# Optimization experiments

Hardware: AMD Instinct MI355X
Metric: run time of the kernel (lower is better)

The kernel has to match this reference:

```python
import jax, jax.numpy as jnp
import numpy as np

N = 100000
E = 1600000
D = 128
LAYERS = 2


def setup_inputs() -> dict:
    key = jax.random.key(0)
    k1, k2, k3, k4, k5, k6 = jax.random.split(key, 6)
    features = jax.random.normal(k1, (N, D), dtype=jnp.float32)
    edge_row = jax.random.randint(k2, (E,), 0, N)
    edge_col = jax.random.randint(k3, (E,), 0, N)
    edge_val = jax.random.uniform(k4, (E,), dtype=jnp.float32)
    # new_features[index] = out_features with out_features having N rows =>
    # index is a permutation covering all N nodes
    index = jax.random.permutation(k5, N)
    a_in = jax.random.normal(k6, (3,), dtype=jnp.float32)
    return {"features": features, "edge_row": edge_row, "edge_col": edge_col,
            "edge_val": edge_val, "index": index, "a_in": a_in}


def reference(features, edge_row, edge_col, edge_val, index, a_in):
    n, d = features.shape
    # --- normalize_adj: D^{-1/2} A D^{-1/2} (Mat is constant across layers) ---
    rowsum = jax.ops.segment_sum(edge_val, edge_row, num_segments=n)  # [N]
    d_inv_sqrt = jnp.where(rowsum > 0, rowsum ** -0.5, 0.0)
    vals = d_inv_sqrt[edge_row] * edge_val * d_inv_sqrt[edge_col]      # [E]

    # softmax over first Layers+1 entries of a_in
    a = jax.nn.softmax(a_in[:LAYERS + 1])

    # nodes covered by index keep the SpMM result; others keep old features
    covered = jnp.zeros((n,), dtype=bool).at[index].set(True)

    result = a[0] * features
    h = features
    for j in range(LAYERS):
        # SpMM: out[r] = sum_e vals[e] * h[col[e]] for row[e] == r
        out = jax.ops.segment_sum(vals[:, None] * h[edge_col], edge_row,
                                  num_segments=n)                      # [N, D]
        scattered = jnp.zeros_like(h).at[index].set(out)
        h = jnp.where(covered[:, None], scattered, h)
        result = result + a[j + 1] * h
    return result
```

## Files before the change

kernel.cpp:

```cpp
#include <hip/hip_runtime.h>

#define WPB    4
#define SCAN_B 1024
#define P1B    256
#define BKT_SH 8

typedef unsigned u32x4 __attribute__((ext_vector_type(4)));
typedef float    f32x4 __attribute__((ext_vector_type(4)));
typedef float    f32x2 __attribute__((ext_vector_type(2)));

__device__ __forceinline__ unsigned bf16rne(float x) {
  unsigned u = __float_as_uint(x);
  return (u + 0x7fffu + ((u >> 16) & 1u)) >> 16;
}
__device__ __forceinline__ float bf_lo(unsigned g) { return __uint_as_float(g << 16); }
__device__ __forceinline__ float bf_hi(unsigned g) { return __uint_as_float(g & 0xffff0000u); }

__global__ void prep_p1_k(const f32x2* __restrict__ f, unsigned* __restrict__ hb, int nw,
                          const float* __restrict__ a_in, float* __restrict__ a_buf,
                          const int* __restrict__ index, int* __restrict__ covered,
                          int* __restrict__ row_start, const int* __restrict__ erow,
                          int* __restrict__ bhist, int E, int N, int C, int NB) {
  extern __shared__ int h[];
  const bool dop1 = (blockIdx.x < P1B);
  if (dop1) {
    for (int k = threadIdx.x; k < NB; k += 256) h[k] = 0;
    __syncthreads();
  }
  int i = blockIdx.x * 256 + threadIdx.x;
  if (i < nw) {
    f32x2 v = __builtin_nontemporal_load(f + i);
    hb[i] = bf16rne(v.x) | (bf16rne(v.y) << 16);
  }
  if (i < N) covered[index[i]] = 1;
  if (i == 0) {
    row_start[N] = E;
    float x0 = a_in[0], x1 = a_in[1], x2 = a_in[2];
    float m = fmaxf(x0, fmaxf(x1, x2));
    float e0 = expf(x0 - m), e1 = expf(x1 - m), e2 = expf(x2 - m);
    float s = e0 + e1 + e2;
    a_buf[0] = e0 / s; a_buf[1] = e1 / s; a_buf[2] = e2 / s;
  }
  if (dop1) {
    int s = blockIdx.x * C, e = min(E, s + C);
    for (int j = s + threadIdx.x; j < e; j += 256)
      atomicAdd(&h[erow[j] >> BKT_SH], 1);
    __syncthreads();
    for (int k = threadIdx.x; k < NB; k += 256)
      bhist[(size_t)k * P1B + blockIdx.x] = h[k];
  }
}

__global__ void scanA_k(const int* __restrict__ cnt, int* __restrict__ incl,
                        int* __restrict__ bsum, int n) {
  __shared__ int tmp[SCAN_B];
  int tid = threadIdx.x;
  int g = blockIdx.x * SCAN_B + tid;
  tmp[tid] = (g < n) ? cnt[g] : 0;
  __syncthreads();
  for (int off = 1; off < SCAN_B; off <<= 1) {
    int t = (tid >= off) ? tmp[tid - off] : 0;
    __syncthreads();
    tmp[tid] += t;
    __syncthreads();
  }
  if (g < n) incl[g] = tmp[tid];
  if (tid == SCAN_B - 1) bsum[blockIdx.x] = tmp[tid];
}

__global__ void scanBC_k(int* __restrict__ boffs, const int* __restrict__ bhist,
                         const int* __restrict__ bsum, int nb, int n) {
  __shared__ int bs[128];
  int tid = threadIdx.x;
  if (tid < 128) bs[tid] = (tid < nb) ? bsum[tid] : 0;
  __syncthreads();
  for (int off = 1; off < 128; off <<= 1) {
    int t = (tid >= off && tid < 128) ? bs[tid - off] : 0;
    __syncthreads();
    if (tid < 128) bs[tid] += t;
    __syncthreads();
  }
  int g = blockIdx.x * SCAN_B + tid;
  if (g < n) {
    int off2 = (blockIdx.x > 0) ? bs[blockIdx.x - 1] : 0;
    boffs[g] = boffs[g] + off2 - bhist[g];
  }
}

__global__ void p2_k(const int* __restrict__ row, const int* __restrict__ col,
                     const float* __restrict__ val, const int* __restrict__ boffs,
                     int2* __restrict__ bedge, int E, int C, int NB) {
  extern __shared__ int cur[];
  for (int k = threadIdx.x; k < NB; k += 256)
    cur[k] = boffs[(size_t)k * P1B + blockIdx.x];
  __syncthreads();
  int s = blockIdx.x * C, e = min(E, s + C);
  for (int i = s + threadIdx.x; i < e; i += 256) {
    int r = row[i];
    int p = atomicAdd(&cur[r >> BKT_SH], 1);
    bedge[p] = make_int2(((r & 255) << 24) | col[i], __float_as_int(val[i]));
  }
}

__global__ void p3_k(const int2* __restrict__ bedge, const int* __restrict__ boffs,
                     int* __restrict__ row_start, float* __restrict__ dis,
                     int2* __restrict__ pairs, int E, int N, int NB) {
  __shared__ int rcnt[256];
  __shared__ float rsum[256];
  __shared__ int rbase[256];
  __shared__ int tmp[256];
  int kb = blockIdx.x, t = threadIdx.x;
  int base = boffs[(size_t)kb * P1B];
  int end  = (kb + 1 < NB) ? boffs[(size_t)(kb + 1) * P1B] : E;
  rcnt[t] = 0; rsum[t] = 0.f;
  __syncthreads();
  for (int i = base + t; i < end; i += 256) {
    int2 p = bedge[i];
    int rlo = ((unsigned)p.x) >> 24;
    atomicAdd(&rcnt[rlo], 1);
    atomicAdd(&rsum[rlo], __int_as_float(p.y));
  }
  __syncthreads();
  int v = rcnt[t];
  tmp[t] = v;
  __syncthreads();
  for (int off = 1; off < 256; off <<= 1) {
    int u = (t >= off) ? tmp[t - off] : 0;
    __syncthreads();
    tmp[t] += u;
    __syncthreads();
  }
  rbase[t] = tmp[t] - v;
  int r = (kb << BKT_SH) + t;
  if (r < N) {
    row_start[r] = base + rbase[t];
    float s = rsum[t];
    dis[r] = (s > 0.0f) ? rsqrtf(s) : 0.0f;
  }
  __syncthreads();
  rcnt[t] = rbase[t];
  __syncthreads();
  for (int i = base + t; i < end; i += 256) {
    int2 p = bedge[i];
    int rlo = ((unsigned)p.x) >> 24;
    int pos = base + atomicAdd(&rcnt[rlo], 1);
    pairs[pos] = make_int2(p.x & 0xFFFFFF, p.y);
  }
}

__device__ __forceinline__ void acc8(float v, u32x4 g, float* a) {
  a[0] = fmaf(v, bf_lo(g.x), a[0]); a[1] = fmaf(v, bf_hi(g.x), a[1]);
  a[2] = fmaf(v, bf_lo(g.y), a[2]); a[3] = fmaf(v, bf_hi(g.y), a[3]);
  a[4] = fmaf(v, bf_lo(g.z), a[4]); a[5] = fmaf(v, bf_hi(g.z), a[5]);
  a[6] = fmaf(v, bf_lo(g.w), a[6]); a[7] = fmaf(v, bf_hi(g.w), a[7]);
}

__device__ __forceinline__ void spmm_body(const int* __restrict__ row_start,
                                          const int2* __restrict__ pairs,
                                          const float* __restrict__ dis,
                                          const char* __restrict__ hb,
                                          int wave, int lane, float* a) {
  int q = lane >> 4;
  unsigned qoff = (unsigned)(lane & 15) << 4;
  int beg = row_start[wave], end = row_start[wave + 1];
  for (int base = beg; base < end; base += 64) {
    unsigned long long pl = 0;
    if (base + lane < end)
      pl = __builtin_nontemporal_load((const unsigned long long*)(pairs + base + lane));
    int pc = (int)(pl & 0xffffffffu);
    float pv = __uint_as_float((unsigned)(pl >> 32)) * dis[pc];
    int m = end - base; if (m > 64) m = 64;
    for (int j = 0; j < m; j += 16) {
      int   c0 = __shfl(pc, j + q),      c1 = __shfl(pc, j + 4 + q);
      int   c2 = __shfl(pc, j + 8 + q),  c3 = __shfl(pc, j + 12 + q);
      float v0 = __shfl(pv, j + q),      v1 = __shfl(pv, j + 4 + q);
      float v2 = __shfl(pv, j + 8 + q),  v3 = __shfl(pv, j + 12 + q);
      u32x4 g0 = *(const u32x4*)(hb + (((unsigned)c0 << 8) | qoff));
      u32x4 g1 = *(const u32x4*)(hb + (((unsigned)c1 << 8) | qoff));
      u32x4 g2 = *(const u32x4*)(hb + (((unsigned)c2 << 8) | qoff));
      u32x4 g3 = *(const u32x4*)(hb + (((unsigned)c3 << 8) | qoff));
      acc8(v0, g0, a); acc8(v1, g1, a);
      acc8(v2, g2, a); acc8(v3, g3, a);
    }
  }
#pragma unroll
  for (int i = 0; i < 8; ++i) a[i] += __shfl_xor(a[i], 16);
#pragma unroll
  for (int i = 0; i < 8; ++i) a[i] += __shfl_xor(a[i], 32);
}

__global__ void spmm1_k(const int* __restrict__ row_start, const int2* __restrict__ pairs,
                        const float* __restrict__ dis, const unsigned* __restrict__ hB,
                        const int* __restrict__ index, u32x4* __restrict__ hA4, int n) {
  int wave = blockIdx.x * WPB + (threadIdx.x >> 6);
  if (wave >= n) return;
  int lane = threadIdx.x & 63;
  float a[8] = {0.f, 0.f, 0.f, 0.f, 0.f, 0.f, 0.f, 0.f};
  spmm_body(row_start, pairs, dis, (const char*)hB, wave, lane, a);
  if ((lane >> 4) == 0) {
    float dr = dis[wave];
    u32x4 pk;
    pk.x = bf16rne(a[0] * dr) | (bf16rne(a[1] * dr) << 16);
    pk.y = bf16rne(a[2] * dr) | (bf16rne(a[3] * dr) << 16);
    pk.z = bf16rne(a[4] * dr) | (bf16rne(a[5] * dr) << 16);
    pk.w = bf16rne(a[6] * dr) | (bf16rne(a[7] * dr) << 16);
    hA4[(unsigned)index[wave] * 16u + (unsigned)(lane & 15)] = pk;
  }
}

__global__ void spmm2_k(const int* __restrict__ row_start, const int2* __restrict__ pairs,
                        const float* __restrict__ dis, const u32x4* __restrict__ hA4,
                        const u32x4* __restrict__ hB4, const int* __restrict__ index,
                        f32x4* __restrict__ out4, const float* __restrict__ ac, int n) {
  int wave = blockIdx.x * WPB + (threadIdx.x >> 6);
  if (wave >= n) return;
  int lane = threadIdx.x & 63;
  float a[8] = {0.f, 0.f, 0.f, 0.f, 0.f, 0.f, 0.f, 0.f};
  spmm_body(row_start, pairs, dis, (const char*)hA4, wave, lane, a);
  if ((lane >> 4) == 0) {
    unsigned ql = lane & 15;
    float dr = dis[wave];
    unsigned ro = (unsigned)index[wave] * 16u + ql;
    u32x4 ga = hA4[ro];
    u32x4 gb = __builtin_nontemporal_load(hB4 + ro);
    float c0 = ac[0], c1 = ac[1], c2 = ac[2];
    f32x4 w0, w1;
    w0.x = fmaf(c2, a[0] * dr, fmaf(c1, bf_lo(ga.x), c0 * bf_lo(gb.x)));
    w0.y = fmaf(c2, a[1] * dr, fmaf(c1, bf_hi(ga.x), c0 * bf_hi(gb.x)));
    w0.z = fmaf(c2, a[2] * dr, fmaf(c1, bf_lo(ga.y), c0 * bf_lo(gb.y)));
    w0.w = fmaf(c2, a[3] * dr, fmaf(c1, bf_hi(ga.y), c0 * bf_hi(gb.y)));
    w1.x = fmaf(c2, a[4] * dr, fmaf(c1, bf_lo(ga.z), c0 * bf_lo(gb.z)));
    w1.y = fmaf(c2, a[5] * dr, fmaf(c1, bf_hi(ga.z), c0 * bf_hi(gb.z)));
    w1.z = fmaf(c2, a[6] * dr, fmaf(c1, bf_lo(ga.w), c0 * bf_lo(gb.w)));
    w1.w = fmaf(c2, a[7] * dr, fmaf(c1, bf_hi(ga.w), c0 * bf_hi(gb.w)));
    unsigned ob = (unsigned)index[wave] * 32u + 2u * ql;
    __builtin_nontemporal_store(w0, out4 + ob);
    __builtin_nontemporal_store(w1, out4 + ob + 1);
  }
}

__global__ void fixup1_k(const int* __restrict__ covered, const u32x4* __restrict__ hB4,
                         u32x4* __restrict__ hA4, int n) {
  int v = blockIdx.x * 256 + threadIdx.x;
  if (v >= n || covered[v]) return;
  for (int d = 0; d < 16; ++d) hA4[(size_t)v * 16 + d] = hB4[(size_t)v * 16 + d];
}

__global__ void fixup2_k(const int* __restrict__ covered, const float2* __restrict__ feat,
                         float2* __restrict__ out, const float* __restrict__ a, int n) {
  int v = blockIdx.x * 256 + threadIdx.x;
  if (v >= n || covered[v]) return;
  float s = a[0] + a[1] + a[2];
  for (int d = 0; d < 64; ++d) {
    float2 f = feat[(size_t)v * 64 + d];
    out[(size_t)v * 64 + d] = make_float2(s * f.x, s * f.y);
  }
}

extern "C" void kernel_launch(void* const* d_in, const int* in_sizes, int n_in,
                              void* d_out, int out_size, void* d_ws, size_t ws_size,
                              hipStream_t stream) {
  const float* features = (const float*)d_in[0];
  const int*   edge_row = (const int*)d_in[1];
  const int*   edge_col = (const int*)d_in[2];
  const float* edge_val = (const float*)d_in[3];
  const int*   index    = (const int*)d_in[4];
  const float* a_in     = (const float*)d_in[5];

  const int E = in_sizes[1];
  const int N = in_sizes[4];
  const int NB = (N + 255) >> BKT_SH;
  const int NBH = NB * P1B;
  const int C = (E + P1B - 1) / P1B;

  float* out = (float*)d_out;

  char* ws = (char*)d_ws;
  size_t off = 0;
  auto carve = [&](size_t bytes) -> char* {
    char* p = ws + off;
    off = (off + bytes + 255) & ~(size_t)255;
    return p;
  };
  float* a_buf     = (float*)carve(16 * sizeof(float));
  float* dis       = (float*)carve((size_t)N * 4);
  int*   covered   = (int*)carve((size_t)N * 4);
  int*   row_start = (int*)carve((size_t)(N + 1) * 4);
  int*   bsum      = (int*)carve(256 * 4);
  int2*  pairs     = (int2*)carve((size_t)E * 8);
  unsigned* hB     = (unsigned*)carve((size_t)N * 64 * 4);
  size_t ov_bytes = (size_t)NBH * 4 * 2 + (size_t)E * 8 + 1024;
  size_t hA_bytes = (size_t)N * 64 * 4;
  char* ovl = carve(ov_bytes > hA_bytes ? ov_bytes : hA_bytes);
  int*  bhist = (int*)ovl;
  int*  boffs = (int*)(ovl + (((size_t)NBH * 4 + 255) & ~(size_t)255));
  int2* bedge = (int2*)(ovl + 2 * (((size_t)NBH * 4 + 255) & ~(size_t)255));
  unsigned* hA = (unsigned*)ovl;
  (void)ws_size; (void)n_in; (void)out_size;

  const int nbW = (N * 64 + 255) / 256;
  const int nbScan = (NBH + SCAN_B - 1) / SCAN_B;
  const int nbN = (N + 255) / 256;
  const size_t ldsB = (size_t)NB * 4;

  hipMemsetAsync(covered, 0, (size_t)N * 4, stream);
  prep_p1_k<<<nbW, 256, ldsB, stream>>>((const f32x2*)features, hB, N * 64,
                                        a_in, a_buf, index, covered, row_start,
                                        edge_row, bhist, E, N, C, NB);
  scanA_k<<<nbScan, SCAN_B, 0, stream>>>(bhist, boffs, bsum, NBH);
  scanBC_k<<<nbScan, SCAN_B, 0, stream>>>(boffs, bhist, bsum, nbScan, NBH);
  p2_k<<<P1B, 256, ldsB, stream>>>(edge_row, edge_col, edge_val, boffs, bedge, E, C, NB);
  p3_k<<<NB, 256, 0, stream>>>(bedge, boffs, row_start, dis, pairs, E, N, NB);

  const int nbSpmm = (N + WPB - 1) / WPB;
  spmm1_k<<<nbSpmm, WPB * 64, 0, stream>>>(row_start, pairs, dis, hB, index,
                                           (u32x4*)hA, N);
  fixup1_k<<<nbN, 256, 0, stream>>>(covered, (const u32x4*)hB, (u32x4*)hA, N);
  spmm2_k<<<nbSpmm, WPB * 64, 0, stream>>>(row_start, pairs, dis, (const u32x4*)hA,
                                           (const u32x4*)hB, index, (f32x4*)out,
                                           a_buf, N);
  fixup2_k<<<nbN, 256, 0, stream>>>(covered, (const float2*)features,
                                    (float2*)out, a_buf, N);
}
```

Before: 212.8 us.

## Assign one 16-lane group per row and sort rows by degree

The SpMM kernels now give each row a 16-lane quarter-wave instead of a full 64-lane wave, which removes the cross-quarter shuffle reduction and the idle lanes on low-degree rows (about 16 edges per row on average). Rows are processed in degree-descending order through a permutation built with a counting sort (histogram, scan, scatter), so the quarter-waves within a wave get similar trip counts. This adds four small preprocessing launches and an indirection through rowperm. It also makes the output scatter and the index reads less coalesced.

```diff
diff --git a/kernel.cpp b/kernel.cpp
--- a/kernel.cpp
+++ b/kernel.cpp
@@ -148,6 +148,35 @@
   }
 }
 
+__global__ void d1_k(const int* __restrict__ row_start, int* __restrict__ dhist,
+                     int N, int CD) {
+  __shared__ int h[256];
+  int t = threadIdx.x;
+  h[t] = 0;
+  __syncthreads();
+  int s = blockIdx.x * CD, e = min(N, s + CD);
+  for (int i = s + t; i < e; i += 256) {
+    int deg = row_start[i + 1] - row_start[i];
+    atomicAdd(&h[255 - min(deg, 255)], 1);
+  }
+  __syncthreads();
+  dhist[(size_t)t * P1B + blockIdx.x] = h[t];
+}
+
+__global__ void d2_k(const int* __restrict__ row_start, const int* __restrict__ doffs,
+                     int* __restrict__ rowperm, int N, int CD) {
+  __shared__ int cur[256];
+  int t = threadIdx.x;
+  cur[t] = doffs[(size_t)t * P1B + blockIdx.x];
+  __syncthreads();
+  int s = blockIdx.x * CD, e = min(N, s + CD);
+  for (int i = s + t; i < e; i += 256) {
+    int deg = row_start[i + 1] - row_start[i];
+    int pos = atomicAdd(&cur[255 - min(deg, 255)], 1);
+    rowperm[pos] = i;
+  }
+}
+
 __device__ __forceinline__ void acc8(float v, u32x4 g, float* a) {
   a[0] = fmaf(v, bf_lo(g.x), a[0]); a[1] = fmaf(v, bf_hi(g.x), a[1]);
   a[2] = fmaf(v, bf_lo(g.y), a[2]); a[3] = fmaf(v, bf_hi(g.y), a[3]);
@@ -159,22 +188,24 @@
                                           const int2* __restrict__ pairs,
                                           const float* __restrict__ dis,
                                           const char* __restrict__ hb,
-                                          int wave, int lane, float* a) {
-  int q = lane >> 4;
-  unsigned qoff = (unsigned)(lane & 15) << 4;
-  int beg = row_start[wave], end = row_start[wave + 1];
-  for (int base = beg; base < end; base += 64) {
+                                          int row, int lane, float* a) {
+  int qbase = lane & ~15;
+  int ql = lane & 15;
+  unsigned qoff = (unsigned)ql << 4;
+  int beg = row_start[row], end = row_start[row + 1];
+  for (int base = beg; base < end; base += 16) {
     unsigned long long pl = 0;
-    if (base + lane < end)
-      pl = __builtin_nontemporal_load((const unsigned long long*)(pairs + base + lane));
+    if (base + ql < end)
+      pl = __builtin_nontemporal_load((const unsigned long long*)(pairs + base + ql));
     int pc = (int)(pl & 0xffffffffu);
     float pv = __uint_as_float((unsigned)(pl >> 32)) * dis[pc];
-    int m = end - base; if (m > 64) m = 64;
-    for (int j = 0; j < m; j += 16) {
-      int   c0 = __shfl(pc, j + q),      c1 = __shfl(pc, j + 4 + q);
-      int   c2 = __shfl(pc, j + 8 + q),  c3 = __shfl(pc, j + 12 + q);
-      float v0 = __shfl(pv, j + q),      v1 = __shfl(pv, j + 4 + q);
-      float v2 = __shfl(pv, j + 8 + q),  v3 = __shfl(pv, j + 12 + q);
+    int m = end - base; if (m > 16) m = 16;
+    int j = 0;
+    for (; j + 4 <= m; j += 4) {
+      int   c0 = __shfl(pc, qbase + j),     c1 = __shfl(pc, qbase + j + 1);
+      int   c2 = __shfl(pc, qbase + j + 2), c3 = __shfl(pc, qbase + j + 3);
+      float v0 = __shfl(pv, qbase + j),     v1 = __shfl(pv, qbase + j + 1);
+      float v2 = __shfl(pv, qbase + j + 2), v3 = __shfl(pv, qbase + j + 3);
       u32x4 g0 = *(const u32x4*)(hb + (((unsigned)c0 << 8) | qoff));
       u32x4 g1 = *(const u32x4*)(hb + (((unsigned)c1 << 8) | qoff));
       u32x4 g2 = *(const u32x4*)(hb + (((unsigned)c2 << 8) | qoff));
@@ -182,61 +213,63 @@
       acc8(v0, g0, a); acc8(v1, g1, a);
       acc8(v2, g2, a); acc8(v3, g3, a);
     }
-  }
-#pragma unroll
-  for (int i = 0; i < 8; ++i) a[i] += __shfl_xor(a[i], 16);
-#pragma unroll
-  for (int i = 0; i < 8; ++i) a[i] += __shfl_xor(a[i], 32);
+    for (; j < m; ++j) {
+      int   c = __shfl(pc, qbase + j);
+      float v = __shfl(pv, qbase + j);
+      u32x4 g = *(const u32x4*)(hb + (((unsigned)c << 8) | qoff));
+      acc8(v, g, a);
+    }
+  }
 }
 
 __global__ void spmm1_k(const int* __restrict__ row_start, const int2* __restrict__ pairs,
                         const float* __restrict__ dis, const unsigned* __restrict__ hB,
-                        const int* __restrict__ index, u32x4* __restrict__ hA4, int n) {
-  int wave = blockIdx.x * WPB + (threadIdx.x >> 6);
-  if (wave >= n) return;
+                        const int* __restrict__ index, const int* __restrict__ rowperm,
+                        u32x4* __restrict__ hA4, int n) {
+  int qid = blockIdx.x * 16 + (threadIdx.x >> 4);
+  if (qid >= n) return;
+  int row = rowperm[qid];
   int lane = threadIdx.x & 63;
   float a[8] = {0.f, 0.f, 0.f, 0.f, 0.f, 0.f, 0.f, 0.f};
-  spmm_body(row_start, pairs, dis, (const char*)hB, wave, lane, a);
-  if ((lane >> 4) == 0) {
-    float dr = dis[wave];
-    u32x4 pk;
-    pk.x = bf16rne(a[0] * dr) | (bf16rne(a[1] * dr) << 16);
-    pk.y = bf16rne(a[2] * dr) | (bf16rne(a[3] * dr) << 16);
-    pk.z = bf16rne(a[4] * dr) | (bf16rne(a[5] * dr) << 16);
-    pk.w = bf16rne(a[6] * dr) | (bf16rne(a[7] * dr) << 16);
-    hA4[(unsigned)index[wave] * 16u + (unsigned)(lane & 15)] = pk;
-  }
+  spmm_body(row_start, pairs, dis, (const char*)hB, row, lane, a);
+  float dr = dis[row];
+  u32x4 pk;
+  pk.x = bf16rne(a[0] * dr) | (bf16rne(a[1] * dr) << 16);
+  pk.y = bf16rne(a[2] * dr) | (bf16rne(a[3] * dr) << 16);
+  pk.z = bf16rne(a[4] * dr) | (bf16rne(a[5] * dr) << 16);
+  pk.w = bf16rne(a[6] * dr) | (bf16rne(a[7] * dr) << 16);
+  hA4[(unsigned)index[row] * 16u + (unsigned)(lane & 15)] = pk;
 }
 
 __global__ void spmm2_k(const int* __restrict__ row_start, const int2* __restrict__ pairs,
                         const float* __restrict__ dis, const u32x4* __restrict__ hA4,
                         const u32x4* __restrict__ hB4, const int* __restrict__ index,
-                        f32x4* __restrict__ out4, const float* __restrict__ ac, int n) {
-  int wave = blockIdx.x * WPB + (threadIdx.x >> 6);
-  if (wave >= n) return;
+                        const int* __restrict__ rowperm, f32x4* __restrict__ out4,
+                        const float* __restrict__ ac, int n) {
+  int qid = blockIdx.x * 16 + (threadIdx.x >> 4);
+  if (qid >= n) return;
+  int row = rowperm[qid];
   int lane = threadIdx.x & 63;
   float a[8] = {0.f, 0.f, 0.f, 0.f, 0.f, 0.f, 0.f, 0.f};
-  spmm_body(row_start, pairs, dis, (const char*)hA4, wave, lane, a);
-  if ((lane >> 4) == 0) {
-    unsigned ql = lane & 15;
-    float dr = dis[wave];
-    unsigned ro = (unsigned)index[wave] * 16u + ql;
-    u32x4 ga = hA4[ro];
-    u32x4 gb = __builtin_nontemporal_load(hB4 + ro);
-    float c0 = ac[0], c1 = ac[1], c2 = ac[2];
-    f32x4 w0, w1;
-    w0.x = fmaf(c2, a[0] * dr, fmaf(c1, bf_lo(ga.x), c0 * bf_lo(gb.x)));
-    w0.y = fmaf(c2, a[1] * dr, fmaf(c1, bf_hi(ga.x), c0 * bf_hi(gb.x)));
-    w0.z = fmaf(c2, a[2] * dr, fmaf(c1, bf_lo(ga.y), c0 * bf_lo(gb.y)));
-    w0.w = fmaf(c2, a[3] * dr, fmaf(c1, bf_hi(ga.y), c0 * bf_hi(gb.y)));
-    w1.x = fmaf(c2, a[4] * dr, fmaf(c1, bf_lo(ga.z), c0 * bf_lo(gb.z)));
-    w1.y = fmaf(c2, a[5] * dr, fmaf(c1, bf_hi(ga.z), c0 * bf_hi(gb.z)));
-    w1.z = fmaf(c2, a[6] * dr, fmaf(c1, bf_lo(ga.w), c0 * bf_lo(gb.w)));
-    w1.w = fmaf(c2, a[7] * dr, fmaf(c1, bf_hi(ga.w), c0 * bf_hi(gb.w)));
-    unsigned ob = (unsigned)index[wave] * 32u + 2u * ql;
-    __builtin_nontemporal_store(w0, out4 + ob);
-    __builtin_nontemporal_store(w1, out4 + ob + 1);
-  }
+  spmm_body(row_start, pairs, dis, (const char*)hA4, row, lane, a);
+  unsigned ql = lane & 15;
+  float dr = dis[row];
+  unsigned ro = (unsigned)index[row] * 16u + ql;
+  u32x4 ga = hA4[ro];
+  u32x4 gb = __builtin_nontemporal_load(hB4 + ro);
+  float c0 = ac[0], c1 = ac[1], c2 = ac[2];
+  f32x4 w0, w1;
+  w0.x = fmaf(c2, a[0] * dr, fmaf(c1, bf_lo(ga.x), c0 * bf_lo(gb.x)));
+  w0.y = fmaf(c2, a[1] * dr, fmaf(c1, bf_hi(ga.x), c0 * bf_hi(gb.x)));
+  w0.z = fmaf(c2, a[2] * dr, fmaf(c1, bf_lo(ga.y), c0 * bf_lo(gb.y)));
+  w0.w = fmaf(c2, a[3] * dr, fmaf(c1, bf_hi(ga.y), c0 * bf_hi(gb.y)));
+  w1.x = fmaf(c2, a[4] * dr, fmaf(c1, bf_lo(ga.z), c0 * bf_lo(gb.z)));
+  w1.y = fmaf(c2, a[5] * dr, fmaf(c1, bf_hi(ga.z), c0 * bf_hi(gb.z)));
+  w1.z = fmaf(c2, a[6] * dr, fmaf(c1, bf_lo(ga.w), c0 * bf_lo(gb.w)));
+  w1.w = fmaf(c2, a[7] * dr, fmaf(c1, bf_hi(ga.w), c0 * bf_hi(gb.w)));
+  unsigned ob = (unsigned)index[row] * 32u + 2u * ql;
+  __builtin_nontemporal_store(w0, out4 + ob);
+  __builtin_nontemporal_store(w1, out4 + ob + 1);
 }
 
 __global__ void fixup1_k(const int* __restrict__ covered, const u32x4* __restrict__ hB4,
@@ -272,6 +305,8 @@
   const int NB = (N + 255) >> BKT_SH;
   const int NBH = NB * P1B;
   const int C = (E + P1B - 1) / P1B;
+  const int CD = (N + P1B - 1) / P1B;
+  const int NDH = 256 * P1B;
 
   float* out = (float*)d_out;
 
@@ -286,20 +321,23 @@
   float* dis       = (float*)carve((size_t)N * 4);
   int*   covered   = (int*)carve((size_t)N * 4);
   int*   row_start = (int*)carve((size_t)(N + 1) * 4);
+  int*   rowperm   = (int*)carve((size_t)N * 4);
   int*   bsum      = (int*)carve(256 * 4);
   int2*  pairs     = (int2*)carve((size_t)E * 8);
   unsigned* hB     = (unsigned*)carve((size_t)N * 64 * 4);
-  size_t ov_bytes = (size_t)NBH * 4 * 2 + (size_t)E * 8 + 1024;
+  size_t tblB = ((size_t)(NBH > NDH ? NBH : NDH) * 4 + 255) & ~(size_t)255;
+  size_t ov_bytes = 2 * tblB + (size_t)E * 8 + 1024;
   size_t hA_bytes = (size_t)N * 64 * 4;
   char* ovl = carve(ov_bytes > hA_bytes ? ov_bytes : hA_bytes);
   int*  bhist = (int*)ovl;
-  int*  boffs = (int*)(ovl + (((size_t)NBH * 4 + 255) & ~(size_t)255));
-  int2* bedge = (int2*)(ovl + 2 * (((size_t)NBH * 4 + 255) & ~(size_t)255));
+  int*  boffs = (int*)(ovl + tblB);
+  int2* bedge = (int2*)(ovl + 2 * tblB);
   unsigned* hA = (unsigned*)ovl;
   (void)ws_size; (void)n_in; (void)out_size;
 
   const int nbW = (N * 64 + 255) / 256;
   const int nbScan = (NBH + SCAN_B - 1) / SCAN_B;
+  const int nbScanD = (NDH + SCAN_B - 1) / SCAN_B;
   const int nbN = (N + 255) / 256;
   const size_t ldsB = (size_t)NB * 4;
 
@@ -311,14 +349,18 @@
   scanBC_k<<<nbScan, SCAN_B, 0, stream>>>(boffs, bhist, bsum, nbScan, NBH);
   p2_k<<<P1B, 256, ldsB, stream>>>(edge_row, edge_col, edge_val, boffs, bedge, E, C, NB);
   p3_k<<<NB, 256, 0, stream>>>(bedge, boffs, row_start, dis, pairs, E, N, NB);
-
-  const int nbSpmm = (N + WPB - 1) / WPB;
-  spmm1_k<<<nbSpmm, WPB * 64, 0, stream>>>(row_start, pairs, dis, hB, index,
-                                           (u32x4*)hA, N);
+  d1_k<<<P1B, 256, 0, stream>>>(row_start, bhist, N, CD);
+  scanA_k<<<nbScanD, SCAN_B, 0, stream>>>(bhist, boffs, bsum, NDH);
+  scanBC_k<<<nbScanD, SCAN_B, 0, stream>>>(boffs, bhist, bsum, nbScanD, NDH);
+  d2_k<<<P1B, 256, 0, stream>>>(row_start, boffs, rowperm, N, CD);
+
+  const int nbSpmm = (N + 15) / 16;
+  spmm1_k<<<nbSpmm, 256, 0, stream>>>(row_start, pairs, dis, hB, index, rowperm,
+                                      (u32x4*)hA, N);
   fixup1_k<<<nbN, 256, 0, stream>>>(covered, (const u32x4*)hB, (u32x4*)hA, N);
-  spmm2_k<<<nbSpmm, WPB * 64, 0, stream>>>(row_start, pairs, dis, (const u32x4*)hA,
-                                           (const u32x4*)hB, index, (f32x4*)out,
-                                           a_buf, N);
+  spmm2_k<<<nbSpmm, 256, 0, stream>>>(row_start, pairs, dis, (const u32x4*)hA,
+                                      (const u32x4*)hB, index, rowperm,
+                                      (f32x4*)out, a_buf, N);
   fixup2_k<<<nbN, 256, 0, stream>>>(covered, (const float2*)features,
                                     (float2*)out, a_buf, N);
 }
```

After: 223.3 us. +4.9%, slower.
